# Optimization experiments

Measured on AMD Instinct MI355X. Metric: run time of the kernel, lower is better.

Reference implementation:

```python
import jax, jax.numpy as jnp
import numpy as np

D_MODEL = 2048
D_LATENT = 512


def setup_inputs() -> dict:
    key = jax.random.key(0)
    ks = jax.random.split(key, 6)
    x = jax.random.normal(ks[0], (2, 4096, D_MODEL), dtype=jnp.float32)
    cache = jax.random.normal(ks[1], (2, 4096, D_LATENT), dtype=jnp.float32)
    s = 0.02
    # weights stored (in_features, out_features); equivalent to torch Linear (no bias)
    W_kv = jax.random.normal(ks[2], (D_MODEL, D_LATENT), dtype=jnp.float32) * s
    W_q = jax.random.normal(ks[3], (D_MODEL, D_MODEL), dtype=jnp.float32) * s
    W_lq = jax.random.normal(ks[4], (D_MODEL, D_LATENT), dtype=jnp.float32) * s
    W_o = jax.random.normal(ks[5], (D_LATENT, D_MODEL), dtype=jnp.float32) * s
    return {"x": x, "cache": cache, "W_kv": W_kv, "W_q": W_q, "W_lq": W_lq, "W_o": W_o}


def reference(x, cache, W_kv, W_q, W_lq, W_o):
    # latent compression of inputs: (B, S, d_latent)
    l_kv_new = jnp.einsum('bsd,dl->bsl', x, W_kv)
    # query path: x -> query (d_model) -> latent query (d_latent)
    q = jnp.einsum('bsd,de->bse', x, W_q)
    lq = jnp.einsum('bse,el->bsl', q, W_lq)
    # append to cache: (B, T+S, d_latent)
    l_kv = jnp.concatenate([cache, l_kv_new], axis=1)
    scale = jnp.sqrt(jnp.float32(D_LATENT)).astype(x.dtype)
    # attention in latent space: scores (B, S, T+S)
    scores = jnp.einsum('bsl,btl->bst', lq, l_kv) / scale
    weights = jax.nn.softmax(scores, axis=-1)
    ctx = jnp.einsum('bst,btl->bsl', weights, l_kv)
    out = jnp.einsum('bsl,ld->bsd', ctx, W_o)
    return out, l_kv
```

## Files before the change

### kernel.cpp

```cpp
#include <hip/hip_runtime.h>
#include <hip/hip_bf16.h>
#include <math.h>


typedef _Float16 f16x8 __attribute__((ext_vector_type(8)));
typedef _Float16 f16x4 __attribute__((ext_vector_type(4)));
typedef float    f32x4 __attribute__((ext_vector_type(4)));
typedef float    f32x8 __attribute__((ext_vector_type(8)));

__device__ __forceinline__ void gl_lds16(const void* g, void* l) {
  __builtin_amdgcn_global_load_lds(
      (const __attribute__((address_space(1))) void*)g,
      (__attribute__((address_space(3))) void*)l, 16, 0, 0);
}


__global__ __launch_bounds__(256) void k_cvt(const float* __restrict__ in,
                                             _Float16* __restrict__ out, int n4) {
  int i = blockIdx.x * blockDim.x + threadIdx.x;
  int st = gridDim.x * blockDim.x;
  for (; i < n4; i += st) {
    f32x4 v = reinterpret_cast<const f32x4*>(in)[i];
    reinterpret_cast<f16x4*>(out)[i] = __builtin_convertvector(v, f16x4);
  }
}

__global__ __launch_bounds__(256) void k_cache(const float* __restrict__ cache,
                                               float* __restrict__ lkv_f32,
                                               _Float16* __restrict__ lkv16, int n4) {
  int i = blockIdx.x * blockDim.x + threadIdx.x;
  int st = gridDim.x * blockDim.x;
  for (; i < n4; i += st) {
    f32x4 v = reinterpret_cast<const f32x4*>(cache)[i];
    int e = i << 2;
    int b = e >> 21;
    int dst = e + (b << 21);
    *reinterpret_cast<f32x4*>(lkv_f32 + dst) = v;
    *reinterpret_cast<f16x4*>(lkv16 + dst) = __builtin_convertvector(v, f16x4);
  }
}

__global__ __launch_bounds__(256) void k_tc(const float* __restrict__ in,
                                            _Float16* __restrict__ out, int R, int C) {
  __shared__ float t[32][33];
  const int c0 = blockIdx.x << 5, r0 = blockIdx.y << 5;
  const int tid = threadIdx.x;
  {
    int r = tid >> 3, c4 = (tid & 7) << 2;
    f32x4 v = *reinterpret_cast<const f32x4*>(&in[(long)(r0 + r) * C + c0 + c4]);
    t[r][c4] = v[0]; t[r][c4 + 1] = v[1]; t[r][c4 + 2] = v[2]; t[r][c4 + 3] = v[3];
  }
  __syncthreads();
  {
    int c = tid >> 3, r4 = (tid & 7) << 2;
    f16x4 o = {(_Float16)t[r4][c], (_Float16)t[r4 + 1][c],
               (_Float16)t[r4 + 2][c], (_Float16)t[r4 + 3][c]};
    *reinterpret_cast<f16x4*>(&out[(long)(c0 + c) * R + r0 + r4]) = o;
  }
}

__global__ __launch_bounds__(256) void k_tb(const _Float16* __restrict__ in,
                                            _Float16* __restrict__ out, int R, int C) {
  __shared__ _Float16 t[32][36];
  const int c0 = blockIdx.x << 5, r0 = blockIdx.y << 5;
  const int tid = threadIdx.x;
  {
    int r = tid >> 3, c4 = (tid & 7) << 2;
    f16x4 v = *reinterpret_cast<const f16x4*>(&in[(long)(r0 + r) * C + c0 + c4]);
    t[r][c4] = v[0]; t[r][c4 + 1] = v[1]; t[r][c4 + 2] = v[2]; t[r][c4 + 3] = v[3];
  }
  __syncthreads();
  {
    int c = tid >> 3, r4 = (tid & 7) << 2;
    f16x4 o = {t[r4][c], t[r4 + 1][c], t[r4 + 2][c], t[r4 + 3][c]};
    *reinterpret_cast<f16x4*>(&out[(long)(c0 + c) * R + r0 + r4]) = o;
  }
}

template <int CMODE>
__global__ __launch_bounds__(256) void k_gemm(const _Float16* __restrict__ A,
                                              const _Float16* __restrict__ B,
                                              float* __restrict__ Cf,
                                              _Float16* __restrict__ Ch,
                                              _Float16* __restrict__ Ch2,
                                              int M, int N, int K, int lda, int ldb,
                                              float cscale) {
  if constexpr (CMODE == 4) {
    const long z = blockIdx.z;
    A += z * K;
    B += z * K;
    Cf += z * (long)M * N;
  }
  __shared__ alignas(16) _Float16 As[128 * 64];
  __shared__ alignas(16) _Float16 Bs[128 * 64];
  const int tid = threadIdx.x;
  const int lane = tid & 63;
  const int w = tid >> 6;
  const int wr = ((w >> 1) & 1) << 6, wc = (w & 1) << 6;
  const int bm = blockIdx.x << 7, bn = blockIdx.y << 7;
  const int g = lane >> 4, ln15 = lane & 15;

  f32x4 acc[4][4] = {};

  const int srowl = lane >> 3;
  const int skcol = (lane & 7) << 3;
  const int wofs = (srowl << 6) + (((lane & 7) ^ srowl) << 3);

  f16x8 ra[4], rb[4];
  auto loadregs = [&](int k0) {
#pragma unroll
    for (int i = 0; i < 4; ++i) {
      int ch = (w << 2) + i;
      int row = (ch << 3) + srowl;
      ra[i] = *reinterpret_cast<const f16x8*>(&A[(long)(bm + row) * lda + k0 + skcol]);
      rb[i] = *reinterpret_cast<const f16x8*>(&B[(long)(bn + row) * ldb + k0 + skcol]);
    }
  };
  loadregs(0);
  const int nk = K >> 6;
  for (int kt = 0; kt < nk; ++kt) {
    __syncthreads();
#pragma unroll
    for (int i = 0; i < 4; ++i) {
      int ch = (w << 2) + i;
      *reinterpret_cast<f16x8*>(&As[(ch << 9) + wofs]) = ra[i];
      *reinterpret_cast<f16x8*>(&Bs[(ch << 9) + wofs]) = rb[i];
    }
    __syncthreads();
    if (kt + 1 < nk) loadregs((kt + 1) << 6);
#pragma unroll
    for (int ks = 0; ks < 2; ++ks) {
      f16x8 af[4], bf[4];
#pragma unroll
      for (int i = 0; i < 4; ++i) {
        const int arow = wr + (i << 4) + ln15;
        const int brow = wc + (i << 4) + ln15;
        const int inner = (((ks << 5) + (g << 3)) ^ ((ln15 & 7) << 3));
        af[i] = *reinterpret_cast<const f16x8*>(&As[arow * 64 + inner]);
        bf[i] = *reinterpret_cast<const f16x8*>(&Bs[brow * 64 + inner]);
      }
#pragma unroll
      for (int i = 0; i < 4; ++i)
#pragma unroll
        for (int j = 0; j < 4; ++j)
          acc[i][j] = __builtin_amdgcn_mfma_f32_16x16x32_f16(af[i], bf[j], acc[i][j], 0, 0, 0);
    }
  }
#pragma unroll
  for (int i = 0; i < 4; ++i) {
    const int row = bm + wr + (i << 4) + (g << 2);
#pragma unroll
    for (int j = 0; j < 4; ++j) {
      const int col = bn + wc + (j << 4) + ln15;
#pragma unroll
      for (int r = 0; r < 4; ++r) {
        float v = acc[i][j][r];
        long orow = row + r;
        if constexpr (CMODE == 2) {
          long m2 = ((orow >> 12) << 13) + 4096 + (orow & 4095);
          Cf[m2 * 512 + col] = v;
          Ch[m2 * 512 + col] = (_Float16)v;
        } else if constexpr (CMODE == 1) {
          Ch[orow * N + col] = (_Float16)v;
        } else if constexpr (CMODE == 3) {
          Ch[orow * N + col] = (_Float16)(v * cscale);
        } else if constexpr (CMODE == 5) {
          if (col < 512) {
            Ch[orow * 512 + col] = (_Float16)v;
          } else {
            long m2 = ((orow >> 12) << 13) + 4096 + (orow & 4095);
            Cf[m2 * 512 + (col - 512)] = v;
            Ch2[m2 * 512 + (col - 512)] = (_Float16)v;
          }
        } else {
          Cf[orow * N + col] = v;
        }
      }
    }
  }
}

template <int CMODE, int STATS>
__global__ __launch_bounds__(512, 2) void k_gemm256(const _Float16* __restrict__ A,
                                                    const _Float16* __restrict__ B,
                                                    float* __restrict__ Cf,
                                                    _Float16* __restrict__ Ch,
                                                    float* __restrict__ Lp,
                                                    int M, int N, int K,
                                                    int lda, int ldb) {
  extern __shared__ _Float16 sm[];
  _Float16* As = sm;
  _Float16* Bs = sm + 32768;
  const int tid = threadIdx.x;
  const int lane = tid & 63;
  const int w = tid >> 6;
  const int wm = w >> 2, wn = w & 3;
  const int bm = blockIdx.x << 8, bn = blockIdx.y << 8;
  const int g = lane >> 4, ln15 = lane & 15;

  f32x4 acc[8][4] = {};

  const int lrow8 = lane >> 3;
  const int lswz  = ((lane & 7) ^ lrow8) << 3;
  const _Float16* Ap[4];
  const _Float16* Bp[4];
  int loff[4];
#pragma unroll
  for (int i = 0; i < 4; ++i) {
    const int row = (i << 6) + (w << 3) + lrow8;
    Ap[i] = &A[(long)(bm + row) * lda + lswz];
    Bp[i] = &B[(long)(bn + row) * ldb + lswz];
    loff[i] = ((i << 6) + (w << 3)) << 6;
  }

  auto stage = [&](int buf, int kt) {
    const int k0 = kt << 6;
    const int bo = buf << 14;
#pragma unroll
    for (int i = 0; i < 4; ++i) {
      gl_lds16(Ap[i] + k0, &As[bo + loff[i]]);
      gl_lds16(Bp[i] + k0, &Bs[bo + loff[i]]);
    }
  };

  const int nk = K >> 6;
  stage(0, 0);
  if (nk > 1) stage(1, 1);

  for (int kt = 0; kt < nk; ++kt) {
    if (kt + 1 < nk) asm volatile("s_waitcnt vmcnt(8)" ::: "memory");
    else             asm volatile("s_waitcnt vmcnt(0)" ::: "memory");
    __builtin_amdgcn_sched_barrier(0);
    __builtin_amdgcn_s_barrier();
    const int bo = (kt & 1) << 14;
#pragma unroll
    for (int ks = 0; ks < 2; ++ks) {
      f16x8 af[8], bf[4];
      const int innersw = ((ks << 5) + (g << 3)) ^ ((ln15 & 7) << 3);
#pragma unroll
      for (int i = 0; i < 8; ++i) {
        const int arow = (wm << 7) + (i << 4) + ln15;
        af[i] = *reinterpret_cast<const f16x8*>(&As[bo + arow * 64 + innersw]);
      }
#pragma unroll
      for (int j = 0; j < 4; ++j) {
        const int brow = (wn << 6) + (j << 4) + ln15;
        bf[j] = *reinterpret_cast<const f16x8*>(&Bs[bo + brow * 64 + innersw]);
      }
#pragma unroll
      for (int i = 0; i < 8; ++i)
#pragma unroll
        for (int j = 0; j < 4; ++j)
          acc[i][j] = __builtin_amdgcn_mfma_f32_16x16x32_f16(af[i], bf[j], acc[i][j], 0, 0, 0);
    }
    asm volatile("s_waitcnt lgkmcnt(0)" ::: "memory");
    __builtin_amdgcn_sched_barrier(0);
    __builtin_amdgcn_s_barrier();
    if (kt + 2 < nk) stage(kt & 1, kt + 2);
  }

  if constexpr (STATS) {
    float* Lsh = (float*)sm;
    float part[8][4];
#pragma unroll
    for (int i = 0; i < 8; ++i) {
      const int row = bm + (wm << 7) + (i << 4) + (g << 2);
#pragma unroll
      for (int r = 0; r < 4; ++r) {
        float s = 0.f;
#pragma unroll
        for (int j = 0; j < 4; ++j) {
          const int col = bn + (wn << 6) + (j << 4) + ln15;
          float e = fminf(__expf(acc[i][j][r]), 60000.f);
          Ch[(long)(row + r) * N + col] = (_Float16)e;
          s += e;
        }
#pragma unroll
        for (int off = 1; off < 16; off <<= 1) s += __shfl_xor(s, off);
        part[i][r] = s;
      }
    }
    if (ln15 == 0) {
#pragma unroll
      for (int i = 0; i < 8; ++i)
#pragma unroll
        for (int r = 0; r < 4; ++r) {
          const int lrow = (wm << 7) + (i << 4) + (g << 2) + r;
          Lsh[(lrow << 2) + wn] = part[i][r];
        }
    }
    __syncthreads();
    if (tid < 256) {
      float L = Lsh[(tid << 2)] + Lsh[(tid << 2) + 1] +
                Lsh[(tid << 2) + 2] + Lsh[(tid << 2) + 3];
      Lp[(long)(bm + tid) * gridDim.y + blockIdx.y] = L;
    }
  } else {
#pragma unroll
    for (int i = 0; i < 8; ++i) {
      const int row = bm + (wm << 7) + (i << 4) + (g << 2);
#pragma unroll
      for (int j = 0; j < 4; ++j) {
        const int col = bn + (wn << 6) + (j << 4) + ln15;
#pragma unroll
        for (int r = 0; r < 4; ++r) {
          if constexpr (CMODE == 1)
            Ch[(long)(row + r) * N + col] = (_Float16)acc[i][j][r];
          else
            Cf[(long)(row + r) * N + col] = acc[i][j][r];
        }
      }
    }
  }
}

__global__ __launch_bounds__(256) void k_linv(const float* __restrict__ Lp,
                                              float* __restrict__ Linv, int nb) {
  const int r = (blockIdx.x << 8) + threadIdx.x;
  float s = 0.f;
  for (int i = 0; i < nb; ++i) s += Lp[(long)r * nb + i];
  Linv[r] = 1.f / s;
}

__global__ __launch_bounds__(256) void k_red4(const float* __restrict__ p,
                                              _Float16* __restrict__ o,
                                              int n4, float scale) {
  const f32x4* pv = reinterpret_cast<const f32x4*>(p);
  int i = blockIdx.x * blockDim.x + threadIdx.x;
  int st = gridDim.x * blockDim.x;
  for (; i < n4; i += st) {
    f32x4 a = pv[i] + pv[i + n4] + pv[i + 2 * n4] + pv[i + 3 * n4];
    a *= scale;
    reinterpret_cast<f16x4*>(o)[i] = __builtin_convertvector(a, f16x4);
  }
}

__global__ __launch_bounds__(256) void k_red4row(const float* __restrict__ p,
                                                 const float* __restrict__ Linv,
                                                 _Float16* __restrict__ o, int n4) {
  const f32x4* pv = reinterpret_cast<const f32x4*>(p);
  int i = blockIdx.x * blockDim.x + threadIdx.x;
  int st = gridDim.x * blockDim.x;
  for (; i < n4; i += st) {
    f32x4 a = pv[i] + pv[i + n4] + pv[i + 2 * n4] + pv[i + 3 * n4];
    a *= Linv[i >> 7];
    reinterpret_cast<f16x4*>(o)[i] = __builtin_convertvector(a, f16x4);
  }
}


extern "C" void kernel_launch(void* const* d_in, const int* in_sizes, int n_in,
                              void* d_out, int out_size, void* d_ws, size_t ws_size,
                              hipStream_t stream) {
  const float* x     = (const float*)d_in[0];
  const float* cache = (const float*)d_in[1];
  const float* W_kv  = (const float*)d_in[2];
  const float* W_q   = (const float*)d_in[3];
  const float* W_lq  = (const float*)d_in[4];
  const float* W_o   = (const float*)d_in[5];

  float* out     = (float*)d_out;
  float* lkv_out = out + (size_t)8192 * 2048;

  _Float16* base16 = (_Float16*)d_out;
  _Float16* x16    = base16;
  _Float16* lq16   = base16 + 16777216;
  _Float16* Wq16   = base16 + 20971520;
  _Float16* WlqT   = base16 + 25165824;
  _Float16* WcombT = base16 + 26214400;
  _Float16* WkvT   = base16 + 27262976;
  _Float16* lkvT16 = base16 + 20971520;
  float*    PVp    = (float*)d_out;
  float*    Lp     = (float*)(base16 + 29360128);
  float*    Linv   = Lp + 131072;

  _Float16* lkv16 = (_Float16*)d_ws;
  _Float16* ctx   = lkv16 + 8388608;
  _Float16* WoT   = ctx + 4194304;
  _Float16* Sbuf  = WoT + 1048576;
  float*    Wcp   = (float*)Sbuf;

  const size_t sbase = 27262976;
  int CR = 1024;
  if (ws_size >= sbase + (size_t)4096 * 8192 * 2) CR = 4096;
  else if (ws_size >= sbase + (size_t)2048 * 8192 * 2) CR = 2048;

  const float iscale = 0.044194173824159216f;

  hipFuncSetAttribute((const void*)k_gemm256<1, 1>,
                      hipFuncAttributeMaxDynamicSharedMemorySize, 131072);
  hipFuncSetAttribute((const void*)k_gemm256<0, 0>,
                      hipFuncAttributeMaxDynamicSharedMemorySize, 131072);

  k_cvt<<<1024, 256, 0, stream>>>(x, x16, 16777216 / 4);
  k_cache<<<1024, 256, 0, stream>>>(cache, lkv_out, lkv16, 4194304 / 4);
  k_tc<<<dim3(16, 64), 256, 0, stream>>>(W_kv, WkvT, 2048, 512);
  k_cvt<<<1024, 256, 0, stream>>>(W_q, Wq16, 4194304 / 4);
  k_tc<<<dim3(16, 64), 256, 0, stream>>>(W_lq, WlqT, 2048, 512);
  k_tc<<<dim3(64, 16), 256, 0, stream>>>(W_o, WoT, 512, 2048);

  k_gemm<4><<<dim3(4, 16, 4), 256, 0, stream>>>(WlqT, Wq16, Wcp, nullptr, nullptr,
                                                512, 2048, 512, 2048, 2048, 1.f);
  k_red4<<<1024, 256, 0, stream>>>(Wcp, WcombT, (512 * 2048) / 4, iscale);
  k_gemm<5><<<dim3(64, 8), 256, 0, stream>>>(x16, WcombT, lkv_out, lq16, lkv16,
                                             8192, 1024, 2048, 2048, 2048, 1.f);
  k_tb<<<dim3(16, 512), 256, 0, stream>>>(lkv16, lkvT16, 16384, 512);

  for (long r0 = 0; r0 < 8192; r0 += CR) {
    const long b = r0 >> 12;
    k_gemm256<1, 1><<<dim3(CR >> 8, 32), 512, 131072, stream>>>(
        lq16 + r0 * 512, lkv16 + b * 8192 * 512, nullptr, Sbuf, Lp,
        CR, 8192, 512, 512, 512);
    k_linv<<<CR >> 8, 256, 0, stream>>>(Lp, Linv, 32);
    k_gemm<4><<<dim3(CR >> 7, 4, 4), 256, 0, stream>>>(
        Sbuf, lkvT16 + b * 8192, PVp, nullptr, nullptr,
        CR, 512, 2048, 8192, 16384, 1.f);
    k_red4row<<<2048, 256, 0, stream>>>(PVp, Linv, ctx + r0 * 512, (CR * 512) / 4);
  }

  k_gemm256<0, 0><<<dim3(32, 8), 512, 131072, stream>>>(ctx, WoT, out, nullptr,
                                                        nullptr,
                                                        8192, 2048, 512, 512, 512);
}
```

Baseline: 337.0 us.

## Fuse fp32-to-fp16 conversion into GEMM loads and store split-K partials as fp16

Removes the standalone conversion kernels for x and W_q. The GEMMs now read fp32 directly and convert to fp16 in registers while loading tiles. The split-K partials of the PV GEMM are also stored as fp16 rather than fp32, which halves that intermediate traffic for the reduce kernel. The costs are wider global loads in the GEMM inner loop and extra rounding error in the fp16 partial sums.

```diff
diff --git a/kernel.cpp b/kernel.cpp
--- a/kernel.cpp
+++ b/kernel.cpp
@@ -12,17 +12,6 @@
   __builtin_amdgcn_global_load_lds(
       (const __attribute__((address_space(1))) void*)g,
       (__attribute__((address_space(3))) void*)l, 16, 0, 0);
-}
-
-
-__global__ __launch_bounds__(256) void k_cvt(const float* __restrict__ in,
-                                             _Float16* __restrict__ out, int n4) {
-  int i = blockIdx.x * blockDim.x + threadIdx.x;
-  int st = gridDim.x * blockDim.x;
-  for (; i < n4; i += st) {
-    f32x4 v = reinterpret_cast<const f32x4*>(in)[i];
-    reinterpret_cast<f16x4*>(out)[i] = __builtin_convertvector(v, f16x4);
-  }
 }
 
 __global__ __launch_bounds__(256) void k_cache(const float* __restrict__ cache,
@@ -77,19 +66,24 @@
   }
 }
 
-template <int CMODE>
-__global__ __launch_bounds__(256) void k_gemm(const _Float16* __restrict__ A,
-                                              const _Float16* __restrict__ B,
+template <int CMODE, int AF32, int BF32>
+__global__ __launch_bounds__(256) void k_gemm(const void* __restrict__ Av,
+                                              const void* __restrict__ Bv,
                                               float* __restrict__ Cf,
                                               _Float16* __restrict__ Ch,
                                               _Float16* __restrict__ Ch2,
                                               int M, int N, int K, int lda, int ldb,
                                               float cscale) {
-  if constexpr (CMODE == 4) {
+  const _Float16* A16 = (const _Float16*)Av;
+  const float*    A32 = (const float*)Av;
+  const _Float16* B16 = (const _Float16*)Bv;
+  const float*    B32 = (const float*)Bv;
+  if constexpr (CMODE == 4 || CMODE == 7) {
     const long z = blockIdx.z;
-    A += z * K;
-    B += z * K;
-    Cf += z * (long)M * N;
+    A16 += z * K; A32 += z * K;
+    B16 += z * K; B32 += z * K;
+    if constexpr (CMODE == 4) Cf += z * (long)M * N;
+    else                      Ch += z * (long)M * N;
   }
   __shared__ alignas(16) _Float16 As[128 * 64];
   __shared__ alignas(16) _Float16 Bs[128 * 64];
@@ -112,8 +106,18 @@
     for (int i = 0; i < 4; ++i) {
       int ch = (w << 2) + i;
       int row = (ch << 3) + srowl;
-      ra[i] = *reinterpret_cast<const f16x8*>(&A[(long)(bm + row) * lda + k0 + skcol]);
-      rb[i] = *reinterpret_cast<const f16x8*>(&B[(long)(bn + row) * ldb + k0 + skcol]);
+      if constexpr (AF32) {
+        f32x8 v = *reinterpret_cast<const f32x8*>(&A32[(long)(bm + row) * lda + k0 + skcol]);
+        ra[i] = __builtin_convertvector(v, f16x8);
+      } else {
+        ra[i] = *reinterpret_cast<const f16x8*>(&A16[(long)(bm + row) * lda + k0 + skcol]);
+      }
+      if constexpr (BF32) {
+        f32x8 v = *reinterpret_cast<const f32x8*>(&B32[(long)(bn + row) * ldb + k0 + skcol]);
+        rb[i] = __builtin_convertvector(v, f16x8);
+      } else {
+        rb[i] = *reinterpret_cast<const f16x8*>(&B16[(long)(bn + row) * ldb + k0 + skcol]);
+      }
     }
   };
   loadregs(0);
@@ -172,6 +176,8 @@
             Cf[m2 * 512 + (col - 512)] = v;
             Ch2[m2 * 512 + (col - 512)] = (_Float16)v;
           }
+        } else if constexpr (CMODE == 7) {
+          Ch[orow * N + col] = (_Float16)v;
         } else {
           Cf[orow * N + col] = v;
         }
@@ -335,14 +341,17 @@
   }
 }
 
-__global__ __launch_bounds__(256) void k_red4row(const float* __restrict__ p,
+__global__ __launch_bounds__(256) void k_red4row(const _Float16* __restrict__ p,
                                                  const float* __restrict__ Linv,
                                                  _Float16* __restrict__ o, int n4) {
-  const f32x4* pv = reinterpret_cast<const f32x4*>(p);
+  const f16x4* pv = reinterpret_cast<const f16x4*>(p);
   int i = blockIdx.x * blockDim.x + threadIdx.x;
   int st = gridDim.x * blockDim.x;
   for (; i < n4; i += st) {
-    f32x4 a = pv[i] + pv[i + n4] + pv[i + 2 * n4] + pv[i + 3 * n4];
+    f32x4 a = __builtin_convertvector(pv[i], f32x4) +
+              __builtin_convertvector(pv[i + n4], f32x4) +
+              __builtin_convertvector(pv[i + 2 * n4], f32x4) +
+              __builtin_convertvector(pv[i + 3 * n4], f32x4);
     a *= Linv[i >> 7];
     reinterpret_cast<f16x4*>(o)[i] = __builtin_convertvector(a, f16x4);
   }
@@ -363,14 +372,12 @@
   float* lkv_out = out + (size_t)8192 * 2048;
 
   _Float16* base16 = (_Float16*)d_out;
-  _Float16* x16    = base16;
   _Float16* lq16   = base16 + 16777216;
-  _Float16* Wq16   = base16 + 20971520;
   _Float16* WlqT   = base16 + 25165824;
   _Float16* WcombT = base16 + 26214400;
   _Float16* WkvT   = base16 + 27262976;
   _Float16* lkvT16 = base16 + 20971520;
-  float*    PVp    = (float*)d_out;
+  _Float16* PVp16  = base16;
   float*    Lp     = (float*)(base16 + 29360128);
   float*    Linv   = Lp + 131072;
 
@@ -392,18 +399,16 @@
   hipFuncSetAttribute((const void*)k_gemm256<0, 0>,
                       hipFuncAttributeMaxDynamicSharedMemorySize, 131072);
 
-  k_cvt<<<1024, 256, 0, stream>>>(x, x16, 16777216 / 4);
   k_cache<<<1024, 256, 0, stream>>>(cache, lkv_out, lkv16, 4194304 / 4);
   k_tc<<<dim3(16, 64), 256, 0, stream>>>(W_kv, WkvT, 2048, 512);
-  k_cvt<<<1024, 256, 0, stream>>>(W_q, Wq16, 4194304 / 4);
   k_tc<<<dim3(16, 64), 256, 0, stream>>>(W_lq, WlqT, 2048, 512);
   k_tc<<<dim3(64, 16), 256, 0, stream>>>(W_o, WoT, 512, 2048);
 
-  k_gemm<4><<<dim3(4, 16, 4), 256, 0, stream>>>(WlqT, Wq16, Wcp, nullptr, nullptr,
-                                                512, 2048, 512, 2048, 2048, 1.f);
+  k_gemm<4, 0, 1><<<dim3(4, 16, 4), 256, 0, stream>>>(
+      WlqT, W_q, Wcp, nullptr, nullptr, 512, 2048, 512, 2048, 2048, 1.f);
   k_red4<<<1024, 256, 0, stream>>>(Wcp, WcombT, (512 * 2048) / 4, iscale);
-  k_gemm<5><<<dim3(64, 8), 256, 0, stream>>>(x16, WcombT, lkv_out, lq16, lkv16,
-                                             8192, 1024, 2048, 2048, 2048, 1.f);
+  k_gemm<5, 1, 0><<<dim3(64, 8), 256, 0, stream>>>(
+      x, WcombT, lkv_out, lq16, lkv16, 8192, 1024, 2048, 2048, 2048, 1.f);
   k_tb<<<dim3(16, 512), 256, 0, stream>>>(lkv16, lkvT16, 16384, 512);
 
   for (long r0 = 0; r0 < 8192; r0 += CR) {
@@ -412,10 +417,10 @@
         lq16 + r0 * 512, lkv16 + b * 8192 * 512, nullptr, Sbuf, Lp,
         CR, 8192, 512, 512, 512);
     k_linv<<<CR >> 8, 256, 0, stream>>>(Lp, Linv, 32);
-    k_gemm<4><<<dim3(CR >> 7, 4, 4), 256, 0, stream>>>(
-        Sbuf, lkvT16 + b * 8192, PVp, nullptr, nullptr,
+    k_gemm<7, 0, 0><<<dim3(CR >> 7, 4, 4), 256, 0, stream>>>(
+        Sbuf, lkvT16 + b * 8192, nullptr, PVp16, nullptr,
         CR, 512, 2048, 8192, 16384, 1.f);
-    k_red4row<<<2048, 256, 0, stream>>>(PVp, Linv, ctx + r0 * 512, (CR * 512) / 4);
+    k_red4row<<<2048, 256, 0, stream>>>(PVp16, Linv, ctx + r0 * 512, (CR * 512) / 4);
   }
 
   k_gemm256<0, 0><<<dim3(32, 8), 512, 131072, stream>>>(ctx, WoT, out, nullptr,
```

New measurement: 336.2 us. About the same (-0.2%).
